# Kernel optimization log

Hardware: AMD Instinct MI355X
Metric: run time of the kernel (lower is better)

The kernel has to match this reference:

```python
import jax, jax.numpy as jnp
import numpy as np

B, S, HID = 2, 2048, 2560
NH, NKV, HD = 8, 4, 256
Q_SIZE, KV_SIZE = NH * HD, NKV * HD
SCALE = 256.0 ** -0.5
SLIDING_WINDOW = 1024 - 1  # config.sliding_window - 1
ROPE_BASE = 10000.0
EPS = 1e-6


def rmsnorm(x, w, eps=EPS):
    xf = x.astype(jnp.float32)
    out = xf * jax.lax.rsqrt(jnp.mean(xf * xf, axis=-1, keepdims=True) + eps)
    return (out * (1.0 + w.astype(jnp.float32))).astype(x.dtype)


def apply_rope(x, positions):
    # x: [B,S,H,D], neox style (rotate halves)
    d = x.shape[-1]
    inv_freq = 1.0 / (ROPE_BASE ** (jnp.arange(0, d, 2, dtype=jnp.float32) / d))
    freqs = positions.astype(jnp.float32)[..., None] * inv_freq  # [B,S,d/2]
    cos = jnp.cos(freqs)[:, :, None, :]
    sin = jnp.sin(freqs)[:, :, None, :]
    x1, x2 = x[..., : d // 2], x[..., d // 2:]
    return jnp.concatenate([x1 * cos - x2 * sin, x2 * cos + x1 * sin], axis=-1).astype(x.dtype)


def setup_inputs() -> dict:
    key = jax.random.key(0)
    ks = jax.random.split(key, 4)
    positions = jnp.broadcast_to(jnp.arange(S, dtype=jnp.int32)[None, :], (B, S))
    hidden_states = jax.random.normal(ks[0], (B, S, HID), dtype=jnp.float32)
    attention_mask = jnp.ones((B, S), dtype=jnp.int32)
    Wqkv = jax.random.normal(ks[1], (HID, Q_SIZE + 2 * KV_SIZE), dtype=jnp.float32) * (HID ** -0.5)
    Wo = jax.random.normal(ks[2], (Q_SIZE, HID), dtype=jnp.float32) * (Q_SIZE ** -0.5)
    q_norm_w = jnp.zeros((HD,), dtype=jnp.float32)
    k_norm_w = jnp.zeros((HD,), dtype=jnp.float32)
    return {"positions": positions, "hidden_states": hidden_states,
            "attention_mask": attention_mask, "Wqkv": Wqkv, "Wo": Wo,
            "q_norm_w": q_norm_w, "k_norm_w": k_norm_w}


def reference(positions, hidden_states, attention_mask, Wqkv, Wo, q_norm_w, k_norm_w):
    b, s, _ = hidden_states.shape
    qkv = hidden_states @ Wqkv
    q, k, v = jnp.split(qkv, [Q_SIZE, Q_SIZE + KV_SIZE], axis=-1)
    q = q.reshape(b, s, NH, HD)
    k = k.reshape(b, s, NKV, HD)
    v = v.reshape(b, s, NKV, HD)
    q = rmsnorm(q, q_norm_w)
    k = rmsnorm(k, k_norm_w)
    q = apply_rope(q, positions)
    k = apply_rope(k, positions)

    # additive mask, replicating source exactly
    idx = jnp.arange(s)
    causal = idx[None, :] > idx[:, None]             # triu(diag=1)
    too_far = (idx[None, :] - idx[:, None]) > SLIDING_WINDOW
    base_mask = causal | too_far                      # [S,S]
    key_pad = attention_mask.astype(bool) == False    # [B,S]
    masked = base_mask[None, None, :, :] | key_pad[:, None, None, :]  # [B,1,S,S]
    add_mask = jnp.where(masked, -jnp.inf, 0.0).astype(jnp.float32)

    # GQA: group queries over kv heads
    g = NH // NKV
    qg = q.reshape(b, s, NKV, g, HD)
    scores = jnp.einsum('bsmgd,btmd->bmgst', qg, k) * SCALE  # [B,NKV,g,S,S]
    scores = scores + add_mask[:, :, None, :, :]
    probs = jax.nn.softmax(scores, axis=-1)
    out = jnp.einsum('bmgst,btmd->bsmgd', probs, v)           # [B,S,NKV,g,HD]
    out = out.reshape(b, s, NH * HD)
    return out @ Wo
```

## Files before the change

### kernel.cpp

```cpp
#include <hip/hip_runtime.h>
#include <stdint.h>

#define S_LEN 2048
#define BATCH 2
#define HIDDEN 2560
#define NH 8
#define NKV 4
#define HD 256
#define QSZ (NH*HD)
#define NQKV 4096
#define MROWS (BATCH*S_LEN)
#define SCALE_ATT 0.0625f

using bf16x8 = __attribute__((__ext_vector_type__(8))) __bf16;
using f32x4  = __attribute__((__ext_vector_type__(4))) float;
using s16x8  = __attribute__((__ext_vector_type__(8))) short;

union B8u { s16x8 s; bf16x8 b; };
union I4B8 { int4 i; bf16x8 b; };

__device__ __forceinline__ unsigned short f2bf(float x){
  unsigned u = __float_as_uint(x);
  u += 0x7fffu + ((u >> 16) & 1u);
  return (unsigned short)(u >> 16);
}
__device__ __forceinline__ bf16x8 ld_bf8(const unsigned short* p){
  B8u u; u.s = *reinterpret_cast<const s16x8*>(p); return u.b;
}
__device__ __forceinline__ f32x4 mfma16(bf16x8 a, bf16x8 b, f32x4 c){
  return __builtin_amdgcn_mfma_f32_16x16x32_bf16(a, b, c, 0, 0, 0);
}
__device__ __forceinline__ void gload16(const void* g, void* l){
  __builtin_amdgcn_global_load_lds((const __attribute__((address_space(1))) void*)g,
                                   (__attribute__((address_space(3))) void*)l,
                                   16, 0, 0);
}
__device__ __forceinline__ int cvtpk(float lo, float hi){
  int r;
  asm("v_cvt_pk_bf16_f32 %0, %1, %2" : "=v"(r) : "v"(lo), "v"(hi));
  return r;
}

__global__ __launch_bounds__(256) void cast_bf16_kernel(
    const float* __restrict__ in, unsigned short* __restrict__ out, int n)
{
  int i = (blockIdx.x * 256 + threadIdx.x) * 4;
  if (i < n){
    float4 v = *reinterpret_cast<const float4*>(in + i);
    ushort4 o;
    o.x = f2bf(v.x); o.y = f2bf(v.y); o.z = f2bf(v.z); o.w = f2bf(v.w);
    *reinterpret_cast<ushort4*>(out + i) = o;
  }
}

__global__ __launch_bounds__(256) void tcast_kernel(
    const float* __restrict__ in, unsigned short* __restrict__ out, int R, int C)
{
  __shared__ float t[32][33];
  int c0 = blockIdx.x * 32, r0 = blockIdx.y * 32;
  int tx = threadIdx.x & 31, ty = threadIdx.x >> 5;
#pragma unroll
  for (int ii = 0; ii < 4; ii++)
    t[ty + ii*8][tx] = in[(size_t)(r0 + ty + ii*8) * C + c0 + tx];
  __syncthreads();
#pragma unroll
  for (int ii = 0; ii < 4; ii++)
    out[(size_t)(c0 + ty + ii*8) * R + r0 + tx] = f2bf(t[tx][ty + ii*8]);
}

__global__ __launch_bounds__(256) void gemm_bt_kernel(
    const unsigned short* __restrict__ A,
    const unsigned short* __restrict__ BT,
    float* __restrict__ C,
    int M, int N, int K)
{
  __shared__ unsigned short As[128 * 32];
  __shared__ unsigned short Bs[128 * 32];
  const int tid  = threadIdx.x;
  const int lane = tid & 63;
  const int wid  = tid >> 6;
  const int bm = blockIdx.y, bn = blockIdx.x;
  const int wm = wid >> 1, wn = wid & 1;
  const int lq = lane & 15, lk = lane >> 4;

  f32x4 acc[4][4] = {};

  const int srow = wid * 32 + (lane >> 2);
  const int scol = (lane & 3) * 8;
  const unsigned short* ag0 = A  + (size_t)(bm*128 + srow     ) * K + scol;
  const unsigned short* ag1 = A  + (size_t)(bm*128 + srow + 16) * K + scol;
  const unsigned short* bg0 = BT + (size_t)(bn*128 + srow     ) * K + scol;
  const unsigned short* bg1 = BT + (size_t)(bn*128 + srow + 16) * K + scol;
  unsigned short* as0 = As + wid * 1024;
  unsigned short* as1 = As + wid * 1024 + 512;
  unsigned short* bs0 = Bs + wid * 1024;
  unsigned short* bs1 = Bs + wid * 1024 + 512;

  const unsigned short* ap = As + (wm*64 + lq) * 32 + lk * 8;
  const unsigned short* bp = Bs + (wn*64 + lq) * 32 + lk * 8;

  for (int k0 = 0; k0 < K; k0 += 32){
    __syncthreads();
    gload16(ag0, as0); gload16(ag1, as1);
    gload16(bg0, bs0); gload16(bg1, bs1);
    ag0 += 32; ag1 += 32; bg0 += 32; bg1 += 32;
    __syncthreads();
    bf16x8 af[4], bfv[4];
#pragma unroll
    for (int i = 0; i < 4; i++){
      af[i]  = ld_bf8(ap + i * 512);
      bfv[i] = ld_bf8(bp + i * 512);
    }
#pragma unroll
    for (int mm = 0; mm < 4; mm++)
#pragma unroll
      for (int nn = 0; nn < 4; nn++)
        acc[mm][nn] = mfma16(af[mm], bfv[nn], acc[mm][nn]);
  }

  const int r0 = bm*128 + wm*64, c0 = bn*128 + wn*64;
#pragma unroll
  for (int mm = 0; mm < 4; mm++)
#pragma unroll
    for (int nn = 0; nn < 4; nn++)
#pragma unroll
      for (int i = 0; i < 4; i++)
        C[(size_t)(r0 + mm*16 + lk*4 + i) * N + (c0 + nn*16 + lq)] = acc[mm][nn][i];
}

__global__ __launch_bounds__(256) void normrope_kernel(
    const float* __restrict__ qkv,
    const int* __restrict__ positions,
    const float* __restrict__ qw, const float* __restrict__ kw,
    unsigned short* __restrict__ qB,
    unsigned short* __restrict__ kB,
    unsigned short* __restrict__ vT)
{
  const int s = blockIdx.x, b = blockIdx.y;
  const int lane = threadIdx.x & 63, wid = threadIdx.x >> 6;
  const float* row = qkv + (size_t)(b * S_LEN + s) * NQKV;
  const float fpos = (float)positions[b * S_LEN + s];

#pragma unroll
  for (int t = 0; t < 4; t++){
    const int seg = t * 4 + wid;
    const int base = seg * HD;
    float x0 = row[base + lane];
    float x1 = row[base + lane + 64];
    float x2 = row[base + lane + 128];
    float x3 = row[base + lane + 192];
    if (seg >= 12){
      const int mh = seg - 12;
      unsigned short* vb = vT + (size_t)(b * NKV + mh) * HD * S_LEN + s;
      vb[(size_t)(lane      ) * S_LEN] = f2bf(x0);
      vb[(size_t)(lane +  64) * S_LEN] = f2bf(x1);
      vb[(size_t)(lane + 128) * S_LEN] = f2bf(x2);
      vb[(size_t)(lane + 192) * S_LEN] = f2bf(x3);
    } else {
      const float* w = (seg < 8) ? qw : kw;
      float ssq = x0*x0 + x1*x1 + x2*x2 + x3*x3;
#pragma unroll
      for (int d = 1; d < 64; d <<= 1) ssq += __shfl_xor(ssq, d, 64);
      float rs = rsqrtf(ssq * (1.0f / 256.0f) + 1e-6f);
      float y0 = x0 * rs * (1.0f + w[lane]);
      float y1 = x1 * rs * (1.0f + w[lane + 64]);
      float y2 = x2 * rs * (1.0f + w[lane + 128]);
      float y3 = x3 * rs * (1.0f + w[lane + 192]);
      const float kln = -9.210340371976184f / 128.0f;
      float inv1 = expf((float)lane * kln);
      float inv2 = expf((float)(lane + 64) * kln);
      float s1, c1, s2, c2;
      sincosf(fpos * inv1, &s1, &c1);
      sincosf(fpos * inv2, &s2, &c2);
      float o0 = y0 * c1 - y2 * s1;
      float o2 = y2 * c1 + y0 * s1;
      float o1 = y1 * c2 - y3 * s2;
      float o3 = y3 * c2 + y1 * s2;
      unsigned short* dst = (seg < 8)
        ? qB + ((size_t)(b * NH  +  seg     ) * S_LEN + s) * HD
        : kB + ((size_t)(b * NKV + (seg - 8)) * S_LEN + s) * HD;
      dst[lane      ] = f2bf(o0);
      dst[lane +  64] = f2bf(o1);
      dst[lane + 128] = f2bf(o2);
      dst[lane + 192] = f2bf(o3);
    }
  }
}

__global__ void maskbits_kernel(const int* __restrict__ amask, unsigned* __restrict__ bm)
{
  int t = threadIdx.x;
  int b = t >> 6, tile = t & 63;
  unsigned m = 0;
  for (int j = 0; j < 32; j++)
    m |= (amask[b * S_LEN + tile * 32 + j] != 0 ? 1u : 0u) << j;
  bm[t] = m;
}

__global__ __launch_bounds__(256) void attn_kernel(
    const unsigned short* __restrict__ qB,
    const unsigned short* __restrict__ kB,
    const unsigned short* __restrict__ vT,
    const unsigned* __restrict__ bmG,
    unsigned short* __restrict__ attnO)
{
  __shared__ unsigned short Kb[2][32 * 256];
  __shared__ unsigned short Vb[2][256 * 32];
  __shared__ unsigned bm_lds[64];

  const int tid  = threadIdx.x;
  const int lane = tid & 63, wid = tid >> 6;
  const int id = blockIdx.x;
  const int mh = id & 3, b = (id >> 2) & 1;
  const int qt = (gridDim.x - 1 - id) >> 3;
  const int h  = mh * 2 + (wid >> 1);
  const int q0 = qt * 32 + (wid & 1) * 16;
  const int lq = lane & 15, lk = lane >> 4;
  const int q  = q0 + lq;

  const unsigned short* qbase = qB + ((size_t)(b * NH + h) * S_LEN + q0 + lq) * HD + lk * 8;
  bf16x8 aq[8];
#pragma unroll
  for (int ks = 0; ks < 8; ks++) aq[ks] = ld_bf8(qbase + ks * 32);

  if (tid < 64) bm_lds[tid] = bmG[(b << 6) + tid];

  const unsigned short* kbase = kB + (size_t)(b * NKV + mh) * S_LEN * HD;
  const unsigned short* vbase = vT + (size_t)(b * NKV + mh) * HD * S_LEN;
  const int krow0 = wid * 2 + (lane >> 5);
  const int kgsrc = (lane & 31) ^ (krow0 & 7);
  const unsigned short* kg0 = kbase + (size_t)krow0 * HD + kgsrc * 8;
  const int vd0 = wid * 16 + (lane >> 2);
  const int vgsrc = (lane & 3) ^ ((lane >> 3) & 3);
  const unsigned short* vg0 = vbase + (size_t)vd0 * S_LEN + vgsrc * 8;

  asm volatile("s_waitcnt vmcnt(0)" ::: "memory");

  float mi = -__builtin_inff(), li = 0.f;
  f32x4 oacc[16] = {};

  const int ktmax = qt * 32;

#define STAGE_K(buf, ktv)                                                      \
  do {                                                                         \
    _Pragma("unroll")                                                          \
    for (int r = 0; r < 4; r++)                                                \
      gload16(kg0 + (size_t)(ktv) * HD + r * (8 * HD),                         \
              &Kb[buf][wid * 512 + r * 2048]);                                 \
  } while (0)
#define STAGE_V(buf, ktv)                                                      \
  do {                                                                         \
    _Pragma("unroll")                                                          \
    for (int r = 0; r < 4; r++)                                                \
      gload16(vg0 + (ktv) + (size_t)r * (64 * S_LEN),                          \
              &Vb[buf][wid * 512 + r * 2048]);                                 \
  } while (0)

  STAGE_K(0, 0);  STAGE_V(0, 0);
  if (ktmax >= 32){ STAGE_K(1, 32); STAGE_V(1, 32); }

  int cur = 0;
  for (int kt = 0; kt <= ktmax; kt += 32, cur ^= 1){
    if (kt < ktmax) asm volatile("s_waitcnt vmcnt(8)" ::: "memory");
    else            asm volatile("s_waitcnt vmcnt(0)" ::: "memory");
    __syncthreads();

    f32x4 s0 = {0.f,0.f,0.f,0.f}, s1 = {0.f,0.f,0.f,0.f};
#pragma unroll
    for (int ks = 0; ks < 8; ks++){
      const int slot = (((ks * 4 + lk) ^ (lq & 7)) << 3);
      bf16x8 kf0 = ld_bf8(&Kb[cur][lq * 256 + slot]);
      bf16x8 kf1 = ld_bf8(&Kb[cur][(16 + lq) * 256 + slot]);
      s0 = mfma16(kf0, aq[ks], s0);
      s1 = mfma16(kf1, aq[ks], s1);
    }

    const unsigned mask32 = bm_lds[kt >> 5];
    const int koff = lk * 4;
    float v0[4], v1[4];
#pragma unroll
    for (int j = 0; j < 4; j++){
      const bool c0 = (kt + koff + j <= q)      && ((mask32 >> (koff + j)) & 1u);
      const bool c1 = (kt + 16 + koff + j <= q) && ((mask32 >> (16 + koff + j)) & 1u);
      v0[j] = c0 ? s0[j] * SCALE_ATT : -__builtin_inff();
      v1[j] = c1 ? s1[j] * SCALE_ATT : -__builtin_inff();
    }
    float tm = fmaxf(fmaxf(fmaxf(v0[0], v0[1]), fmaxf(v0[2], v0[3])),
                     fmaxf(fmaxf(v1[0], v1[1]), fmaxf(v1[2], v1[3])));
    tm = fmaxf(tm, __shfl_xor(tm, 16, 64));
    tm = fmaxf(tm, __shfl_xor(tm, 32, 64));

    float p0[4], p1[4];
    if (__all(tm <= mi + 8.0f)){
      const float mns = fmaxf(mi, -1e30f);
#pragma unroll
      for (int j = 0; j < 4; j++){
        p0[j] = __expf(v0[j] - mns);
        p1[j] = __expf(v1[j] - mns);
      }
      float rs = (p0[0] + p0[1]) + (p0[2] + p0[3]) + (p1[0] + p1[1]) + (p1[2] + p1[3]);
      rs += __shfl_xor(rs, 16, 64);
      rs += __shfl_xor(rs, 32, 64);
      li += rs;
    } else {
      const float mn  = fmaxf(mi, tm);
      const float mns = fmaxf(mn, -1e30f);
#pragma unroll
      for (int j = 0; j < 4; j++){
        p0[j] = __expf(v0[j] - mns);
        p1[j] = __expf(v1[j] - mns);
      }
      const float a_ = __expf(mi - mns);
      float rs = (p0[0] + p0[1]) + (p0[2] + p0[3]) + (p1[0] + p1[1]) + (p1[2] + p1[3]);
      rs += __shfl_xor(rs, 16, 64);
      rs += __shfl_xor(rs, 32, 64);
      li = li * a_ + rs;
      mi = mn;
      float av[4];
#pragma unroll
      for (int i = 0; i < 4; i++)
        av[i] = __shfl(a_, (lane & 48) | (lk * 4 + i), 64);
#pragma unroll
      for (int db = 0; db < 16; db++){
        f32x4 o = oacc[db];
#pragma unroll
        for (int i = 0; i < 4; i++) o[i] *= av[i];
        oacc[db] = o;
      }
    }

    const int w0 = cvtpk(p0[0], p0[1]), w1 = cvtpk(p0[2], p0[3]);
    const int w2 = cvtpk(p1[0], p1[1]), w3 = cvtpk(p1[2], p1[3]);
    const int sA = (((lk & 1) * 2) << 4) | lq;
    const int sB = sA + 16;
    const int a0 = __shfl(w0, sA, 64), a1 = __shfl(w1, sA, 64);
    const int b0 = __shfl(w0, sB, 64), b1 = __shfl(w1, sB, 64);
    const int c0w = __shfl(w2, sA, 64), c1w = __shfl(w3, sA, 64);
    const int d0w = __shfl(w2, sB, 64), d1w = __shfl(w3, sB, 64);
    const bool hi = (lk >= 2);
    I4B8 pau;
    pau.i.x = hi ? c0w : a0;
    pau.i.y = hi ? c1w : a1;
    pau.i.z = hi ? d0w : b0;
    pau.i.w = hi ? d1w : b1;

    const int vslot = (lk ^ ((lq >> 1) & 3)) << 3;
#pragma unroll
    for (int db = 0; db < 16; db++){
      bf16x8 vf = ld_bf8(&Vb[cur][(db * 16 + lq) * 32 + vslot]);
      oacc[db] = mfma16(pau.b, vf, oacc[db]);
    }

    __syncthreads();
    if (kt + 64 <= ktmax){ STAGE_K(cur, kt + 64); STAGE_V(cur, kt + 64); }
  }
#undef STAGE_K
#undef STAGE_V

#pragma unroll
  for (int i = 0; i < 4; i++){
    const float lf = __shfl(li, (lane & 48) | (lk * 4 + i), 64);
    const float inv = 1.0f / lf;
    unsigned short* orow = attnO + (size_t)(b * S_LEN + q0 + lk*4 + i) * QSZ + h * HD + lq;
#pragma unroll
    for (int db = 0; db < 16; db++)
      orow[db * 16] = f2bf(oacc[db][i] * inv);
  }
}

extern "C" void kernel_launch(void* const* d_in, const int* in_sizes, int n_in,
                              void* d_out, int out_size, void* d_ws, size_t ws_size,
                              hipStream_t stream)
{
  const int*   positions = (const int*)  d_in[0];
  const float* hidden    = (const float*)d_in[1];
  const int*   amask     = (const int*)  d_in[2];
  const float* Wqkv      = (const float*)d_in[3];
  const float* Wo        = (const float*)d_in[4];
  const float* qw        = (const float*)d_in[5];
  const float* kw        = (const float*)d_in[6];
  float* out = (float*)d_out;

  char* ws = (char*)d_ws;
  unsigned short* hB    = (unsigned short*)(ws);
  unsigned short* attnO = (unsigned short*)(ws);
  unsigned short* WqT   = (unsigned short*)(ws + 20971520);
  unsigned short* WoT   = (unsigned short*)(ws + 41943040);
  float*          qkvF  = (float*)        (ws + 52428800);
  unsigned short* qb    = (unsigned short*)(ws + 119537664);
  unsigned short* kb    = (unsigned short*)(ws + 136314880);
  unsigned short* vt    = (unsigned short*)(ws + 144703488);
  unsigned*       bm    = (unsigned*)     (ws + 153092096);

  cast_bf16_kernel<<<dim3(MROWS * HIDDEN / 1024), 256, 0, stream>>>(hidden, hB, MROWS * HIDDEN);
  tcast_kernel<<<dim3(NQKV / 32, HIDDEN / 32), 256, 0, stream>>>(Wqkv, WqT, HIDDEN, NQKV);
  tcast_kernel<<<dim3(HIDDEN / 32, QSZ / 32), 256, 0, stream>>>(Wo, WoT, QSZ, HIDDEN);
  maskbits_kernel<<<dim3(1), 128, 0, stream>>>(amask, bm);

  gemm_bt_kernel<<<dim3(NQKV / 128, MROWS / 128), 256, 0, stream>>>(hB, WqT, qkvF, MROWS, NQKV, HIDDEN);

  normrope_kernel<<<dim3(S_LEN, BATCH), 256, 0, stream>>>(qkvF, positions, qw, kw, qb, kb, vt);

  attn_kernel<<<dim3(S_LEN / 32 * NKV * BATCH), 256, 0, stream>>>(qb, kb, vt, bm, attnO);

  gemm_bt_kernel<<<dim3(HIDDEN / 128, MROWS / 128), 256, 0, stream>>>(attnO, WoT, out, MROWS, HIDDEN, QSZ);
}
```

Baseline: 383.8 us.

## Replace 128x128 GEMM with double-buffered 256x256 tile pipelined kernel

Both projection GEMMs now use a new kernel with 256x256 output tiles, 512 threads, a 64-wide K step, and double-buffered LDS. Async global-to-LDS loads for the next tile are interleaved with MFMA quarters under explicit vmcnt waits and barriers. LDS uses an XOR swizzle to avoid bank conflicts, workgroups are remapped in an XCD-aware way, and MFMA sections raise wave priority. The goal is to hide memory latency and increase data reuse in the GEMMs. In exchange it uses far more LDS and registers, and a small grid (for example 160 blocks for the output projection) may underfill the GPU.

After: 352.9 us. 1.09x faster.

```diff
diff --git a/kernel.cpp b/kernel.cpp
--- a/kernel.cpp
+++ b/kernel.cpp
@@ -68,64 +68,110 @@
     out[(size_t)(c0 + ty + ii*8) * R + r0 + tx] = f2bf(t[tx][ty + ii*8]);
 }
 
-__global__ __launch_bounds__(256) void gemm_bt_kernel(
+__global__ __launch_bounds__(512, 2) void gemm256_kernel(
     const unsigned short* __restrict__ A,
     const unsigned short* __restrict__ BT,
     float* __restrict__ C,
-    int M, int N, int K)
-{
-  __shared__ unsigned short As[128 * 32];
-  __shared__ unsigned short Bs[128 * 32];
+    int N, int K, int nbn)
+{
+  __shared__ unsigned short Ab[2][256 * 64];
+  __shared__ unsigned short Bb[2][256 * 64];
+
   const int tid  = threadIdx.x;
   const int lane = tid & 63;
   const int wid  = tid >> 6;
-  const int bm = blockIdx.y, bn = blockIdx.x;
-  const int wm = wid >> 1, wn = wid & 1;
+  const int wm = wid >> 2, wn = wid & 3;
   const int lq = lane & 15, lk = lane >> 4;
 
-  f32x4 acc[4][4] = {};
-
-  const int srow = wid * 32 + (lane >> 2);
-  const int scol = (lane & 3) * 8;
-  const unsigned short* ag0 = A  + (size_t)(bm*128 + srow     ) * K + scol;
-  const unsigned short* ag1 = A  + (size_t)(bm*128 + srow + 16) * K + scol;
-  const unsigned short* bg0 = BT + (size_t)(bn*128 + srow     ) * K + scol;
-  const unsigned short* bg1 = BT + (size_t)(bn*128 + srow + 16) * K + scol;
-  unsigned short* as0 = As + wid * 1024;
-  unsigned short* as1 = As + wid * 1024 + 512;
-  unsigned short* bs0 = Bs + wid * 1024;
-  unsigned short* bs1 = Bs + wid * 1024 + 512;
-
-  const unsigned short* ap = As + (wm*64 + lq) * 32 + lk * 8;
-  const unsigned short* bp = Bs + (wn*64 + lq) * 32 + lk * 8;
-
-  for (int k0 = 0; k0 < K; k0 += 32){
-    __syncthreads();
-    gload16(ag0, as0); gload16(ag1, as1);
-    gload16(bg0, bs0); gload16(bg1, bs1);
-    ag0 += 32; ag1 += 32; bg0 += 32; bg1 += 32;
-    __syncthreads();
-    bf16x8 af[4], bfv[4];
-#pragma unroll
-    for (int i = 0; i < 4; i++){
-      af[i]  = ld_bf8(ap + i * 512);
-      bfv[i] = ld_bf8(bp + i * 512);
-    }
-#pragma unroll
-    for (int mm = 0; mm < 4; mm++)
-#pragma unroll
-      for (int nn = 0; nn < 4; nn++)
-        acc[mm][nn] = mfma16(af[mm], bfv[nn], acc[mm][nn]);
-  }
-
-  const int r0 = bm*128 + wm*64, c0 = bn*128 + wn*64;
-#pragma unroll
-  for (int mm = 0; mm < 4; mm++)
-#pragma unroll
-    for (int nn = 0; nn < 4; nn++)
-#pragma unroll
-      for (int i = 0; i < 4; i++)
-        C[(size_t)(r0 + mm*16 + lk*4 + i) * N + (c0 + nn*16 + lq)] = acc[mm][nn][i];
+  const int cpx = gridDim.x >> 3;
+  const int wg  = (blockIdx.x & 7) * cpx + (blockIdx.x >> 3);
+  const int bm = wg / nbn, bn = wg % nbn;
+
+  const int l8 = lane >> 3;
+  const int sl = ((lane & 7) ^ l8) * 8;
+  const unsigned short* agS = A  + (size_t)(bm*256 + wid*16 + l8) * K + sl;
+  const unsigned short* bgS = BT + (size_t)(bn*256 + wid*16 + l8) * K + sl;
+
+  f32x4 acc[4][4][2] = {};
+  bf16x8 a[4][2], b[2][2];
+
+#define STA(c, h, tt) do {                                                    \
+    unsigned short* d = &Ab[c][(h)*8192 + wid*1024];                          \
+    const unsigned short* s = agS + (size_t)(h)*128*K + (size_t)(tt)*64;      \
+    gload16(s, d); gload16(s + 8*(size_t)K, d + 512);                         \
+  } while (0)
+#define STB(c, h, tt) do {                                                    \
+    unsigned short* d = &Bb[c][(h)*8192 + wid*1024];                          \
+    const unsigned short* s = bgS + (size_t)(h)*128*K + (size_t)(tt)*64;      \
+    gload16(s, d); gload16(s + 8*(size_t)K, d + 512);                         \
+  } while (0)
+#define LDA(qa) do {                                                          \
+    _Pragma("unroll") for (int m = 0; m < 4; m++)                             \
+    _Pragma("unroll") for (int kk = 0; kk < 2; kk++)                          \
+      a[m][kk] = ld_bf8(&Ab[cur][((qa)*128 + wm*64 + m*16 + lq)*64            \
+                                 + (((kk*4 + lk) ^ (lq & 7)) << 3)]);         \
+  } while (0)
+#define LDB(qb) do {                                                          \
+    _Pragma("unroll") for (int n = 0; n < 2; n++)                             \
+    _Pragma("unroll") for (int kk = 0; kk < 2; kk++)                          \
+      b[n][kk] = ld_bf8(&Bb[cur][((qb)*128 + wn*32 + n*16 + lq)*64            \
+                                 + (((kk*4 + lk) ^ (lq & 7)) << 3)]);         \
+  } while (0)
+#define MM(qi) do {                                                           \
+    __builtin_amdgcn_s_setprio(1);                                            \
+    _Pragma("unroll") for (int m = 0; m < 4; m++)                             \
+    _Pragma("unroll") for (int n = 0; n < 2; n++)                             \
+    _Pragma("unroll") for (int kk = 0; kk < 2; kk++)                          \
+      acc[qi][m][n] = mfma16(a[m][kk], b[n][kk], acc[qi][m][n]);              \
+    __builtin_amdgcn_s_setprio(0);                                            \
+  } while (0)
+#define BARR __builtin_amdgcn_s_barrier()
+#define VM(n) asm volatile("s_waitcnt vmcnt(" #n ")" ::: "memory")
+
+  STA(0, 0, 0); STB(0, 0, 0); STB(0, 1, 0); STA(0, 1, 0);
+  VM(4); BARR;
+
+  const int NT = K >> 6;
+  for (int t = 0; t < NT - 1; ++t){
+    const int cur = t & 1, nxt = cur ^ 1;
+    LDA(0); LDB(0); STA(nxt, 0, t+1);
+    BARR; MM(0); VM(4); BARR;
+    LDB(1);         STB(nxt, 0, t+1);
+    BARR; MM(1); VM(4); BARR;
+    LDA(1);         STB(nxt, 1, t+1);
+    BARR; MM(2);        BARR;
+    LDB(0);         STA(nxt, 1, t+1);
+    BARR; MM(3); VM(4); BARR;
+  }
+  {
+    const int cur = (NT - 1) & 1;
+    LDA(0); LDB(0); BARR; MM(0); VM(2); BARR;
+    LDB(1);         BARR; MM(1); VM(0); BARR;
+    LDA(1);         BARR; MM(2);        BARR;
+    LDB(0);         BARR; MM(3);        BARR;
+  }
+#undef STA
+#undef STB
+#undef LDA
+#undef LDB
+#undef MM
+#undef BARR
+#undef VM
+
+#pragma unroll
+  for (int qi = 0; qi < 4; qi++){
+    const int qa = qi >> 1;
+    const int qb = (qi ^ (qi >> 1)) & 1;
+    const int r0 = bm*256 + qa*128 + wm*64;
+    const int c0 = bn*256 + qb*128 + wn*32;
+#pragma unroll
+    for (int m = 0; m < 4; m++)
+#pragma unroll
+      for (int n = 0; n < 2; n++)
+#pragma unroll
+        for (int i = 0; i < 4; i++)
+          C[(size_t)(r0 + m*16 + lk*4 + i) * N + (c0 + n*16 + lq)] = acc[qi][m][n][i];
+  }
 }
 
 __global__ __launch_bounds__(256) void normrope_kernel(
@@ -397,11 +443,13 @@
   tcast_kernel<<<dim3(HIDDEN / 32, QSZ / 32), 256, 0, stream>>>(Wo, WoT, QSZ, HIDDEN);
   maskbits_kernel<<<dim3(1), 128, 0, stream>>>(amask, bm);
 
-  gemm_bt_kernel<<<dim3(NQKV / 128, MROWS / 128), 256, 0, stream>>>(hB, WqT, qkvF, MROWS, NQKV, HIDDEN);
+  gemm256_kernel<<<dim3((MROWS/256) * (NQKV/256)), 512, 0, stream>>>(
+      hB, WqT, qkvF, NQKV, HIDDEN, NQKV/256);
 
   normrope_kernel<<<dim3(S_LEN, BATCH), 256, 0, stream>>>(qkvF, positions, qw, kw, qb, kb, vt);
 
   attn_kernel<<<dim3(S_LEN / 32 * NKV * BATCH), 256, 0, stream>>>(qb, kb, vt, bm, attnO);
 
-  gemm_bt_kernel<<<dim3(HIDDEN / 128, MROWS / 128), 256, 0, stream>>>(attnO, WoT, out, MROWS, HIDDEN, QSZ);
-}
+  gemm256_kernel<<<dim3((MROWS/256) * (HIDDEN/256)), 512, 0, stream>>>(
+      attnO, WoT, out, HIDDEN, QSZ, HIDDEN/256);
+}
```
